# Kernel tuning notes

Measured on AMD Instinct MI355X. Metric: run time of the kernel, lower is better.

## Reference

```python
import jax, jax.numpy as jnp
import numpy as np

H = 64          # hidden_dim
EP = 60000      # edges per relation type; block order: nmos, pmos, R, L, C
E = 5 * EP
N_IN = 50000
N_OUT = 50000


def _gelu(x):
    return jax.nn.gelu(x, approximate=False)  # torch nn.GELU default = exact erf


def _mlp_blocked(x, Ws, bs):
    # x: [T, N, Din]; independent MLP per relation-type block; GELU after all but last layer
    for i, (W, b) in enumerate(zip(Ws, bs)):
        x = jnp.einsum('tnd,tdh->tnh', x, W) + b[:, None, :]
        if i < len(Ws) - 1:
            x = _gelu(x)
    return x


def _mlp(x, Ws, bs):
    for i, (W, b) in enumerate(zip(Ws, bs)):
        x = x @ W + b
        if i < len(Ws) - 1:
            x = _gelu(x)
    return x


def _segment_softmax(logits, seg, num_seg):
    # torch_geometric-style softmax: normalized per dst-node segment, per feature column
    m = jax.ops.segment_max(logits, seg, num_segments=num_seg)
    ex = jnp.exp(logits - m[seg])
    den = jax.ops.segment_sum(ex, seg, num_segments=num_seg)
    return ex / den[seg]


def _forward(floats, src_types, dst_types, src_nodes, dst_nodes,
             vg_types, vg_idx, vb_types, vb_idx, n_output_nodes):
    (input_voltages, device_params, nf1_W, nf1_b,
     ef1_W1, ef1_b1, ef1_W2, ef1_b2, ef1_W3, ef1_b3,
     ef2m_W1, ef2m_b1, ef2m_W2, ef2m_b2, ef2m_W3, ef2m_b3, ef2m_W4, ef2m_b4,
     ef2r_W1, ef2r_b1, ef2r_W2, ef2r_b2, ef2r_W3, ef2r_b3, ef2r_W4, ef2r_b4,
     self_W1, self_b1, self_W2, self_b2, self_W3, self_b3, self_W4, self_b4,
     score_W, score_b) = floats
    # ef1: per-relation-type 3-layer MLP on the scalar device parameter -> [E, H]
    ef1 = _mlp_blocked(device_params,
                       [ef1_W1, ef1_W2, ef1_W3],
                       [ef1_b1, ef1_b2, ef1_b3]).reshape(E, H)
    nf1_input = input_voltages[:, None] @ nf1_W + nf1_b           # [N_IN, H]
    # (ef1 @ ef1.T)[dst_out] @ ef1 == ef1[dst_out] @ (ef1.T @ ef1) -- avoids the E x E matrix
    logits = ef1 @ (ef1.T @ ef1)                                  # [E, H]
    # edges whose dst is not an 'output' node go to a dump segment that is dropped
    seg = jnp.where(dst_types == 1, dst_nodes, n_output_nodes)
    att = _segment_softmax(logits, seg, n_output_nodes + 1)
    nf1_output = jax.ops.segment_sum(att * ef1, seg,
                                     num_segments=n_output_nodes + 1)[:n_output_nodes]

    def pick(types, idx):
        # node_types.index: 0 -> 'input' table, 1 -> 'output' table
        return jnp.where((types == 0)[:, None], nf1_input[idx], nf1_output[idx])

    nf1_src = pick(src_types, src_nodes)
    nf1_dst = pick(dst_types, dst_nodes)
    nf1_vg = pick(vg_types, vg_idx)     # gate node feats (mos edges only) [2*EP, H]
    nf1_vb = pick(vb_types, vb_idx)     # bulk node feats (mos edges only) [2*EP, H]

    M = 2 * EP
    x_mos = jnp.concatenate([ef1[:M], nf1_src[:M], nf1_dst[:M], nf1_vg, nf1_vb], -1).reshape(2, EP, 5 * H)
    x_rlc = jnp.concatenate([ef1[M:], nf1_src[M:], nf1_dst[M:]], -1).reshape(3, EP, 3 * H)
    ef2_mos = _mlp_blocked(x_mos, [ef2m_W1, ef2m_W2, ef2m_W3, ef2m_W4],
                           [ef2m_b1, ef2m_b2, ef2m_b3, ef2m_b4])
    ef2_rlc = _mlp_blocked(x_rlc, [ef2r_W1, ef2r_W2, ef2r_W3, ef2r_W4],
                           [ef2r_b1, ef2r_b2, ef2r_b3, ef2r_b4])
    ef2 = jnp.concatenate([ef2_mos.reshape(M, H), ef2_rlc.reshape(3 * EP, H)], 0)
    ef2 = ef2 + _mlp(ef1, [self_W1, self_W2, self_W3, self_W4],
                     [self_b1, self_b2, self_b3, self_b4])
    return ef2 @ score_W + score_b                                # [E, H]


def setup_inputs():
    key = jax.random.key(0)
    ks = iter(jax.random.split(key, 64))

    def nrm(shape, s):
        return jax.random.normal(next(ks), shape, jnp.float32) * s

    def ri(shape, hi):
        return jax.random.randint(next(ks), shape, 0, hi, jnp.int32)

    w = 0.1  # ~ xavier-normal scale for these fan-ins
    return {
        'input_voltages': nrm([N_IN], 1.0),
        'device_params': nrm([5, EP, 1], 1.0),
        'src_types': ri([E], 2), 'dst_types': ri([E], 2),
        'src_nodes': ri([E], N_IN), 'dst_nodes': ri([E], N_OUT),
        'vg_types': ri([2 * EP], 2), 'vg_idx': ri([2 * EP], N_IN),
        'vb_types': ri([2 * EP], 2), 'vb_idx': ri([2 * EP], N_IN),
        'n_output_nodes': N_OUT,
        'nf1_W': nrm([1, H], w), 'nf1_b': nrm([H], w),
        'ef1_W1': nrm([5, 1, H], w), 'ef1_b1': nrm([5, H], w),
        'ef1_W2': nrm([5, H, H], w), 'ef1_b2': nrm([5, H], w),
        'ef1_W3': nrm([5, H, H], w), 'ef1_b3': nrm([5, H], w),
        'ef2m_W1': nrm([2, 5 * H, H], 0.05), 'ef2m_b1': nrm([2, H], w),
        'ef2m_W2': nrm([2, H, H], w), 'ef2m_b2': nrm([2, H], w),
        'ef2m_W3': nrm([2, H, H], w), 'ef2m_b3': nrm([2, H], w),
        'ef2m_W4': nrm([2, H, H], w), 'ef2m_b4': nrm([2, H], w),
        'ef2r_W1': nrm([3, 3 * H, H], 0.05), 'ef2r_b1': nrm([3, H], w),
        'ef2r_W2': nrm([3, H, H], w), 'ef2r_b2': nrm([3, H], w),
        'ef2r_W3': nrm([3, H, H], w), 'ef2r_b3': nrm([3, H], w),
        'ef2r_W4': nrm([3, H, H], w), 'ef2r_b4': nrm([3, H], w),
        'self_W1': nrm([H, H], w), 'self_b1': nrm([H], w),
        'self_W2': nrm([H, H], w), 'self_b2': nrm([H], w),
        'self_W3': nrm([H, H], w), 'self_b3': nrm([H], w),
        'self_W4': nrm([H, H], w), 'self_b4': nrm([H], w),
        'score_W': nrm([H, H], w), 'score_b': nrm([H], w),
    }


def reference(input_voltages, device_params, src_types, dst_types, src_nodes, dst_nodes,
              vg_types, vg_idx, vb_types, vb_idx, n_output_nodes,
              nf1_W, nf1_b,
              ef1_W1, ef1_b1, ef1_W2, ef1_b2, ef1_W3, ef1_b3,
              ef2m_W1, ef2m_b1, ef2m_W2, ef2m_b2, ef2m_W3, ef2m_b3, ef2m_W4, ef2m_b4,
              ef2r_W1, ef2r_b1, ef2r_W2, ef2r_b2, ef2r_W3, ef2r_b3, ef2r_W4, ef2r_b4,
              self_W1, self_b1, self_W2, self_b2, self_W3, self_b3, self_W4, self_b4,
              score_W, score_b):
    floats = (input_voltages, device_params, nf1_W, nf1_b,
              ef1_W1, ef1_b1, ef1_W2, ef1_b2, ef1_W3, ef1_b3,
              ef2m_W1, ef2m_b1, ef2m_W2, ef2m_b2, ef2m_W3, ef2m_b3, ef2m_W4, ef2m_b4,
              ef2r_W1, ef2r_b1, ef2r_W2, ef2r_b2, ef2r_W3, ef2r_b3, ef2r_W4, ef2r_b4,
              self_W1, self_b1, self_W2, self_b2, self_W3, self_b3, self_W4, self_b4,
              score_W, score_b)
    return _forward(floats, src_types, dst_types, src_nodes, dst_nodes,
                    vg_types, vg_idx, vb_types, vb_idx, n_output_nodes)
```

## Files before the change

kernel.cpp:

```cpp
#include <hip/hip_runtime.h>
#include <hip/hip_bf16.h>

#define EP 60000
#define NE 300000
#define M2 120000
#define NIN 50000
#define NOUT 50000
#define PAD 65
#define NIMG 49
#define GP 72

typedef __bf16 b16x8 __attribute__((ext_vector_type(8)));
typedef float f32x4 __attribute__((ext_vector_type(4)));
typedef unsigned short us8 __attribute__((ext_vector_type(8)));
typedef unsigned short us4 __attribute__((ext_vector_type(4)));

__device__ __forceinline__ float gelu_f(float x) {
    return 0.5f * x * (1.0f + erff(x * 0.70710678118654752440f));
}

__device__ __forceinline__ float gelu_fast(float x) {
    float ax = fabsf(x) * 0.70710678118654752440f;
    float t = __builtin_amdgcn_rcpf(fmaf(0.3275911f, ax, 1.0f));
    float y = fmaf(fmaf(fmaf(fmaf(1.061405429f, t, -1.453152027f), t, 1.421413741f),
                        t, -0.284496736f), t, 0.254829592f) * t;
    float e = __expf(-ax * ax);
    float erf = fmaf(-y, e, 1.0f);
    return 0.5f * x * (1.0f + copysignf(erf, x));
}

__device__ __forceinline__ unsigned short bfhi(float f) {
    unsigned int u = __float_as_uint(f);
    u += 0x7FFFu + ((u >> 16) & 1u);
    return (unsigned short)(u >> 16);
}

__device__ __forceinline__ void split2(float f, unsigned short& h, unsigned short& l) {
    h = bfhi(f);
    float fh = __uint_as_float(((unsigned int)h) << 16);
    l = bfhi(f - fh);
}

__device__ __forceinline__ void split2f(float f, unsigned short& h, unsigned short& l) {
    unsigned int u = __float_as_uint(f);
    h = (unsigned short)(u >> 16);
    float fh = __uint_as_float(u & 0xFFFF0000u);
    l = bfhi(f - fh);
}

__device__ __forceinline__ float bf2f(unsigned short u) {
    return __uint_as_float(((unsigned int)u) << 16);
}

__device__ __forceinline__ int xidx(int row, int col) {
    return (row * 64 + col) ^ ((row & 7) << 3);
}

__device__ __forceinline__ b16x8 ldfrag(const unsigned short* p, int id) {
    return __builtin_bit_cast(b16x8, *(const us8*)(p + id));
}

__device__ __forceinline__ f32x4 MF(b16x8 a, b16x8 b, f32x4 c) {
    return __builtin_amdgcn_mfma_f32_16x16x32_bf16(a, b, c, 0, 0, 0);
}

__device__ __forceinline__ void zacc(f32x4 a[2][2]) {
#pragma unroll
    for (int i = 0; i < 2; ++i)
#pragma unroll
        for (int j = 0; j < 2; ++j) a[i][j] = (f32x4){0.f, 0.f, 0.f, 0.f};
}

__device__ __forceinline__ void gll16(const unsigned short* g, unsigned short* l) {
    __builtin_amdgcn_global_load_lds((const __attribute__((address_space(1))) void*)g,
                                     (__attribute__((address_space(3))) void*)l, 16, 0, 0);
}

__device__ __forceinline__ void stageWimg(const unsigned short* __restrict__ img,
                                          unsigned short* __restrict__ WHL, int tid) {
    int w = tid >> 6, lane = tid & 63;
#pragma unroll
    for (int j = 0; j < 2; ++j)
        gll16(img + w * 1024 + j * 512 + lane * 8, WHL + w * 1024 + j * 512);
}

__device__ __forceinline__ void stageX_rows(const unsigned short* __restrict__ src, int rmax,
                                            unsigned short* __restrict__ XH, unsigned short* __restrict__ XL,
                                            int tid) {
#pragma unroll
    for (int q = 0; q < 4; ++q) {
        int f = q * 512 + tid;
        int row = f >> 4, cc = f & 15;
        int rc = min(row, rmax - 1);
        us8 v = *(const us8*)(src + (size_t)rc * 128 + cc * 8);
        unsigned short* pl = (cc < 8) ? XH : XL;
        *(us8*)(pl + xidx(row, (cc & 7) * 8)) = v;
    }
}

__device__ __forceinline__ void stageX_pick(const int* __restrict__ tp, const int* __restrict__ ix, int base,
                                            int rmax, const float* __restrict__ volt,
                                            const unsigned short* __restrict__ nfo,
                                            const float* __restrict__ sNW, const float* __restrict__ sNB,
                                            unsigned short* __restrict__ XH, unsigned short* __restrict__ XL,
                                            int tid) {
#pragma unroll
    for (int q = 0; q < 4; ++q) {
        int f = q * 512 + tid;
        int row = f >> 4, cc = f & 15;
        int rc = min(row, rmax - 1);
        int ty = tp[base + rc];
        int idx = ix[base + rc];
        int c8 = (cc & 7) * 8;
        unsigned short* pl = (cc < 8) ? XH : XL;
        us8 v;
        if (ty == 0) {
            float vv = volt[idx];
#pragma unroll
            for (int j = 0; j < 8; ++j) {
                float x = fmaf(vv, sNW[c8 + j], sNB[c8 + j]);
                unsigned short h, l;
                split2f(x, h, l);
                v[j] = (cc < 8) ? h : l;
            }
        } else {
            v = *(const us8*)(nfo + (size_t)idx * 128 + cc * 8);
        }
        *(us8*)(pl + xidx(row, c8)) = v;
    }
}

__device__ __forceinline__ void mf_gemm64(const unsigned short* __restrict__ XH, const unsigned short* __restrict__ XL,
                                          const unsigned short* __restrict__ WH, const unsigned short* __restrict__ WL,
                                          f32x4 acc[2][2], int wr, int wc, int lane) {
    int lr = lane & 15, g = lane >> 4;
#pragma unroll
    for (int kk = 0; kk < 2; ++kk) {
        int k0 = kk * 32 + g * 8;
        b16x8 ah[2], al[2];
#pragma unroll
        for (int rt = 0; rt < 2; ++rt) {
            int id = xidx(wr * 32 + rt * 16 + lr, k0);
            ah[rt] = ldfrag(XH, id);
            al[rt] = ldfrag(XL, id);
        }
#pragma unroll
        for (int t = 0; t < 2; ++t) {
            int id = xidx((wc * 2 + t) * 16 + lr, k0);
            b16x8 bh = ldfrag(WH, id), bl = ldfrag(WL, id);
#pragma unroll
            for (int rt = 0; rt < 2; ++rt) {
                acc[rt][t] = MF(ah[rt], bh, acc[rt][t]);
                acc[rt][t] = MF(ah[rt], bl, acc[rt][t]);
                acc[rt][t] = MF(al[rt], bh, acc[rt][t]);
            }
        }
    }
}

template <bool GELU, bool FAST>
__device__ __forceinline__ void writeback(f32x4 acc[2][2], const float* __restrict__ sb,
                                          unsigned short* __restrict__ XH, unsigned short* __restrict__ XL,
                                          int wr, int wc, int lane) {
    int lr = lane & 15, g = lane >> 4;
#pragma unroll
    for (int rt = 0; rt < 2; ++rt)
#pragma unroll
        for (int t = 0; t < 2; ++t)
#pragma unroll
            for (int r = 0; r < 4; ++r) {
                int row = wr * 32 + rt * 16 + g * 4 + r;
                int col = (wc * 2 + t) * 16 + lr;
                float v = acc[rt][t][r] + sb[col];
                if (GELU) v = FAST ? gelu_fast(v) : gelu_f(v);
                unsigned short h, l;
                if (FAST) split2f(v, h, l); else split2(v, h, l);
                int id = xidx(row, col);
                XH[id] = h; XL[id] = l;
            }
}

__device__ __forceinline__ void writeglob(f32x4 acc[2][2], const float* __restrict__ sb,
                                          float* __restrict__ dst, int rmax, int wr, int wc, int lane) {
    int lr = lane & 15, g = lane >> 4;
#pragma unroll
    for (int rt = 0; rt < 2; ++rt)
#pragma unroll
        for (int t = 0; t < 2; ++t)
#pragma unroll
            for (int r = 0; r < 4; ++r) {
                int row = wr * 32 + rt * 16 + g * 4 + r;
                if (row < rmax) {
                    int col = (wc * 2 + t) * 16 + lr;
                    dst[(size_t)row * 64 + col] = acc[rt][t][r] + sb[col];
                }
            }
}

__device__ __forceinline__ void writeglob_split(f32x4 acc[2][2], const float* __restrict__ sb,
                                                unsigned short* __restrict__ dst, int rmax,
                                                int wr, int wc, int lane) {
    int lr = lane & 15, g = lane >> 4;
#pragma unroll
    for (int rt = 0; rt < 2; ++rt)
#pragma unroll
        for (int t = 0; t < 2; ++t)
#pragma unroll
            for (int r = 0; r < 4; ++r) {
                int row = wr * 32 + rt * 16 + g * 4 + r;
                if (row < rmax) {
                    int col = (wc * 2 + t) * 16 + lr;
                    float v = acc[rt][t][r] + sb[col];
                    unsigned short h, l;
                    split2(v, h, l);
                    dst[(size_t)row * 128 + col] = h;
                    dst[(size_t)row * 128 + 64 + col] = l;
                }
            }
}

__global__ void k_zero(int* __restrict__ p, int n) {
    int i = blockIdx.x * 256 + threadIdx.x;
    if (i < n) p[i] = 0;
}

__global__ __launch_bounds__(256) void k_prepw(
    const float* __restrict__ e1W2, const float* __restrict__ e1W3,
    const float* __restrict__ mW1, const float* __restrict__ mW2,
    const float* __restrict__ mW3, const float* __restrict__ mW4,
    const float* __restrict__ rW1, const float* __restrict__ rW2,
    const float* __restrict__ rW3, const float* __restrict__ rW4,
    const float* __restrict__ sw1, const float* __restrict__ sw2,
    const float* __restrict__ sw3, const float* __restrict__ sw4,
    const float* __restrict__ scw, unsigned short* __restrict__ wimg) {
    int b = blockIdx.x, tid = threadIdx.x;
    const float* src;
    if (b < 5) src = e1W2 + b * 4096;
    else if (b < 10) src = e1W3 + (b - 5) * 4096;
    else if (b < 20) src = mW1 + (b - 10) * 4096;
    else if (b < 22) src = mW2 + (b - 20) * 4096;
    else if (b < 24) src = mW3 + (b - 22) * 4096;
    else if (b < 26) src = mW4 + (b - 24) * 4096;
    else if (b < 35) src = rW1 + (b - 26) * 4096;
    else if (b < 38) src = rW2 + (b - 35) * 4096;
    else if (b < 41) src = rW3 + (b - 38) * 4096;
    else if (b < 44) src = rW4 + (b - 41) * 4096;
    else if (b == 44) src = sw1;
    else if (b == 45) src = sw2;
    else if (b == 46) src = sw3;
    else if (b == 47) src = sw4;
    else src = scw;
    unsigned short* dst = wimg + (size_t)b * 8192;
#pragma unroll
    for (int q = 0; q < 4; ++q) {
        int flat = q * 256 + tid;
        int k = flat >> 4, n4 = (flat & 15) * 4;
        float4 v = ((const float4*)src)[flat];
        float vv[4] = {v.x, v.y, v.z, v.w};
#pragma unroll
        for (int i = 0; i < 4; ++i) {
            unsigned short h, l;
            split2(vv[i], h, l);
            int id = xidx(n4 + i, k);
            dst[id] = h;
            dst[4096 + id] = l;
        }
    }
}

__global__ __launch_bounds__(512, 4) void k_ef1(
    const float* __restrict__ dp,
    const float* __restrict__ w1, const float* __restrict__ b1,
    const float* __restrict__ b2, const float* __restrict__ b3,
    const unsigned short* __restrict__ wimg,
    unsigned short* __restrict__ e1s) {
    __shared__ unsigned short XH[8192], XL[8192], WHL[8192];
    __shared__ float sb[2][64], sW1[64], sB1[64];
    const int tid = threadIdx.x, ty = blockIdx.y;
    const int i0 = blockIdx.x * 128;
    const int rmax = min(128, EP - i0);
    const int w = tid >> 6, lane = tid & 63;
    const int wr = w >> 1, wc = w & 1;
    const size_t row0 = (size_t)ty * EP + i0;

    stageWimg(wimg + (size_t)ty * 8192, WHL, tid);
    if (tid < 64) { sW1[tid] = w1[ty * 64 + tid]; sB1[tid] = b1[ty * 64 + tid]; }
    else if (tid < 128) sb[0][tid - 64] = b2[ty * 64 + tid - 64];
    else if (tid < 192) sb[1][tid - 128] = b3[ty * 64 + tid - 128];
    __syncthreads();
#pragma unroll
    for (int q = 0; q < 4; ++q) {
        int flat = q * 512 + tid;
        int rr = flat >> 4, cc = flat & 15;
        int rc = min(rr, rmax - 1);
        float d = dp[(size_t)ty * EP + i0 + rc];
        us4 h, l;
#pragma unroll
        for (int j = 0; j < 4; ++j) {
            int c = cc * 4 + j;
            float v = gelu_f(fmaf(d, sW1[c], sB1[c]));
            unsigned short hh, ll;
            split2(v, hh, ll);
            h[j] = hh; l[j] = ll;
        }
        *(us4*)(XH + xidx(rr, cc * 4)) = h;
        *(us4*)(XL + xidx(rr, cc * 4)) = l;
    }
    __syncthreads();
    f32x4 acc[2][2];
    zacc(acc); mf_gemm64(XH, XL, WHL, WHL + 4096, acc, wr, wc, lane);
    __syncthreads();
    writeback<true, false>(acc, sb[0], XH, XL, wr, wc, lane);
    stageWimg(wimg + (size_t)(5 + ty) * 8192, WHL, tid);
    __syncthreads();
    zacc(acc); mf_gemm64(XH, XL, WHL, WHL + 4096, acc, wr, wc, lane);
    writeglob_split(acc, sb[1], e1s + row0 * 128, rmax, wr, wc, lane);
}

__device__ __forceinline__ void zero16(float* a) {
#pragma unroll
    for (int q = 0; q < 16; ++q) a[q] = 0.f;
}

__device__ __forceinline__ void stage4k(const float* __restrict__ g, float* __restrict__ l) {
    const float4* g4 = (const float4*)g;
    float4* l4 = (float4*)l;
    int t = threadIdx.x;
#pragma unroll
    for (int q = 0; q < 4; ++q) l4[q * 256 + t] = g4[q * 256 + t];
}

__device__ __forceinline__ void tile_gemm(const float* __restrict__ xt, const float* __restrict__ Wl,
                                          float* __restrict__ acc, int r, int c4) {
    const float4* W4 = (const float4*)Wl;
#pragma unroll 8
    for (int k = 0; k < 64; ++k) {
        float xv = xt[r * PAD + k];
#pragma unroll
        for (int q = 0; q < 4; ++q) {
            float4 w = W4[k * 16 + c4 + q];
            acc[q * 4 + 0] = fmaf(xv, w.x, acc[q * 4 + 0]);
            acc[q * 4 + 1] = fmaf(xv, w.y, acc[q * 4 + 1]);
            acc[q * 4 + 2] = fmaf(xv, w.z, acc[q * 4 + 2]);
            acc[q * 4 + 3] = fmaf(xv, w.w, acc[q * 4 + 3]);
        }
    }
}

__global__ __launch_bounds__(256) void k_gram(const unsigned short* __restrict__ e1s, float* __restrict__ G) {
    __shared__ unsigned short TH[64 * GP], TL[64 * GP];
    const int tid = threadIdx.x;
    const int wv = tid >> 6, lane = tid & 63;
    const int lr = lane & 15, g = lane >> 4;
    f32x4 acc[4];
#pragma unroll
    for (int t = 0; t < 4; ++t) acc[t] = (f32x4){0.f, 0.f, 0.f, 0.f};
    const int nchk = (NE + 63) >> 6;
    for (int ch = blockIdx.x; ch < nchk; ch += gridDim.x) {
        int r0 = ch * 64;
        __syncthreads();
#pragma unroll
        for (int q = 0; q < 4; ++q) {
            int f = q * 256 + tid;
            int pl = f >> 9, rem = f & 511;
            int row = rem >> 3, cc = rem & 7;
            int rr = r0 + row;
            us8 v = (us8){0, 0, 0, 0, 0, 0, 0, 0};
            if (rr < NE) v = *(const us8*)(e1s + (size_t)rr * 128 + pl * 64 + cc * 8);
            unsigned short* dstp = pl ? TL : TH;
#pragma unroll
            for (int j = 0; j < 8; ++j) dstp[(cc * 8 + j) * GP + row] = v[j];
        }
        __syncthreads();
#pragma unroll
        for (int kk = 0; kk < 2; ++kk) {
            int k0 = kk * 32 + g * 8;
            b16x8 ah = ldfrag(TH, (wv * 16 + lr) * GP + k0);
            b16x8 al = ldfrag(TL, (wv * 16 + lr) * GP + k0);
#pragma unroll
            for (int b = 0; b < 4; ++b) {
                b16x8 bh = ldfrag(TH, (b * 16 + lr) * GP + k0);
                b16x8 bl = ldfrag(TL, (b * 16 + lr) * GP + k0);
                acc[b] = MF(ah, bh, acc[b]);
                acc[b] = MF(ah, bl, acc[b]);
                acc[b] = MF(al, bh, acc[b]);
            }
        }
    }
#pragma unroll
    for (int b = 0; b < 4; ++b)
#pragma unroll
        for (int r = 0; r < 4; ++r) {
            int row = wv * 16 + g * 4 + r;
            int col = b * 16 + lr;
            atomicAdd(&G[row * 64 + col], acc[b][r]);
        }
}

__global__ void k_hist(const int* __restrict__ dst_t, const int* __restrict__ dst_n, int* __restrict__ hist) {
    int e = blockIdx.x * 256 + threadIdx.x;
    if (e < NE && dst_t[e] == 1) atomicAdd(&hist[dst_n[e]], 1);
}

__global__ __launch_bounds__(1024) void k_scan(const int* __restrict__ hist, int* __restrict__ row_start) {
    __shared__ int part[1024];
    const int tid = threadIdx.x;
    const int chunk = (NOUT + 1023) / 1024;
    int lo = tid * chunk, hi = min(lo + chunk, NOUT);
    int s = 0;
    for (int i = lo; i < hi; ++i) s += hist[i];
    part[tid] = s;
    __syncthreads();
    for (int off = 1; off < 1024; off <<= 1) {
        int v = part[tid];
        int add = (tid >= off) ? part[tid - off] : 0;
        __syncthreads();
        part[tid] = v + add;
        __syncthreads();
    }
    int base = (tid == 0) ? 0 : part[tid - 1];
    for (int i = lo; i < hi; ++i) { row_start[i] = base; base += hist[i]; }
    if (lo < NOUT && hi == NOUT) row_start[NOUT] = base;
}

__global__ void k_scatter(const int* __restrict__ dst_t, const int* __restrict__ dst_n,
                          const int* __restrict__ row_start, int* __restrict__ cursor, int* __restrict__ elist) {
    int e = blockIdx.x * 256 + threadIdx.x;
    if (e < NE && dst_t[e] == 1) {
        int n = dst_n[e];
        int pos = atomicAdd(&cursor[n], 1);
        elist[row_start[n] + pos] = e;
    }
}

__global__ __launch_bounds__(256) void k_logits_c(const unsigned short* __restrict__ e1s,
                                                  const float* __restrict__ G,
                                                  const int* __restrict__ row_start,
                                                  const int* __restrict__ elist,
                                                  float* __restrict__ lgc) {
    __shared__ float A[64 * PAD], Wb[4096];
    const int tid = threadIdx.x;
    const int NV = row_start[NOUT];
    const int i0 = blockIdx.x * 64;
    if (i0 >= NV) return;
    const int rmax = min(64, NV - i0);
    const int r = tid & 63, c0 = (tid >> 6) * 16, c4 = c0 >> 2;
    stage4k(G, Wb);
#pragma unroll
    for (int q = 0; q < 4; ++q) {
        int flat = q * 256 + tid;
        int rr = flat >> 4, cc = flat & 15;
        int rc = min(rr, rmax - 1);
        int eid = elist[i0 + rc];
        const unsigned short* rp = e1s + (size_t)eid * 128;
        us4 h = *(const us4*)(rp + cc * 4);
        us4 l = *(const us4*)(rp + 64 + cc * 4);
        float* d = &A[rr * PAD + cc * 4];
#pragma unroll
        for (int j = 0; j < 4; ++j) d[j] = bf2f(h[j]) + bf2f(l[j]);
    }
    __syncthreads();
    float acc[16];
    zero16(acc); tile_gemm(A, Wb, acc, r, c4);
    if (r < rmax) {
        float* dst = lgc + (size_t)(i0 + r) * 64;
#pragma unroll
        for (int q = 0; q < 4; ++q)
            ((float4*)dst)[c4 + q] =
                make_float4(acc[q * 4 + 0], acc[q * 4 + 1], acc[q * 4 + 2], acc[q * 4 + 3]);
    }
}

__global__ __launch_bounds__(256) void k_att(const float* __restrict__ lgc, const unsigned short* __restrict__ e1s,
                                             const int* __restrict__ row_start, const int* __restrict__ elist,
                                             unsigned short* __restrict__ nfo) {
    int n = blockIdx.x * 4 + (threadIdx.x >> 6);
    int lane = threadIdx.x & 63;
    if (n >= NOUT) return;
    int s = row_start[n], t = row_start[n + 1];
    float m = -3.0e38f, den = 0.f, num = 0.f;
    for (int i = s; i < t; ++i) {
        int eid = elist[i];
        float x = lgc[(size_t)i * 64 + lane];
        float e = bf2f(e1s[(size_t)eid * 128 + lane]) + bf2f(e1s[(size_t)eid * 128 + 64 + lane]);
        float mn = fmaxf(m, x);
        float sc = __expf(m - mn);
        float ex = __expf(x - mn);
        den = fmaf(den, sc, ex);
        num = fmaf(num, sc, ex * e);
        m = mn;
    }
    float v = (t > s) ? num / den : 0.f;
    unsigned short h, l;
    split2(v, h, l);
    nfo[(size_t)n * 128 + lane] = h;
    nfo[(size_t)n * 128 + 64 + lane] = l;
}

__global__ __launch_bounds__(512, 4) void k_fuse(
    const unsigned short* __restrict__ e1s, const unsigned short* __restrict__ nfo,
    const unsigned short* __restrict__ wimg, const float* __restrict__ volt,
    const int* __restrict__ src_t, const int* __restrict__ src_n,
    const int* __restrict__ dst_t, const int* __restrict__ dst_n,
    const int* __restrict__ vg_t, const int* __restrict__ vg_i,
    const int* __restrict__ vb_t, const int* __restrict__ vb_i,
    const float* __restrict__ nf1W, const float* __restrict__ nf1b,
    const float* __restrict__ mb1, const float* __restrict__ mb2,
    const float* __restrict__ mb3, const float* __restrict__ mb4,
    const float* __restrict__ rb1, const float* __restrict__ rb2,
    const float* __restrict__ rb3, const float* __restrict__ rb4,
    const float* __restrict__ selb1, const float* __restrict__ selb2,
    const float* __restrict__ selb3, const float* __restrict__ selb4,
    const float* __restrict__ scb, float* __restrict__ out) {
    __shared__ unsigned short XH[8192], XL[8192], WHL[8192];
    __shared__ float sb[3][64], sNW[64], sNB[64];
    const int tid = threadIdx.x;
    const int gy = blockIdx.y;
    const bool mos = gy < 2;
    const int ty = mos ? gy : gy - 2;
    const int nch = mos ? 5 : 3;
    const int i0 = blockIdx.x * 128;
    const int rmax = min(128, EP - i0);
    const int w = tid >> 6, lane = tid & 63;
    const int wr = w >> 1, wc = w & 1;
    const int lr = lane & 15;
    const int erow0 = (mos ? 0 : M2) + ty * EP + i0;
    const int w1base = mos ? 10 + ty * 5 : 26 + ty * 3;
    const int w2img = mos ? 20 + ty : 35 + ty;
    const int w3img = mos ? 22 + ty : 38 + ty;
    const int w4img = mos ? 24 + ty : 41 + ty;
    const float* b1 = mos ? mb1 : rb1;
    const float* b2 = mos ? mb2 : rb2;
    const float* b3 = mos ? mb3 : rb3;
    const float* b4 = mos ? mb4 : rb4;

    stageWimg(wimg + (size_t)44 * 8192, WHL, tid);
    stageX_rows(e1s + (size_t)erow0 * 128, rmax, XH, XL, tid);
    if (tid < 64) sNW[tid] = nf1W[tid];
    else if (tid < 128) sNB[tid - 64] = nf1b[tid - 64];
    else if (tid < 192) sb[0][tid - 128] = b1[ty * 64 + tid - 128];
    __syncthreads();

    f32x4 acc[2][2], accS[2][2], ef2r[2][2];
    zacc(accS);
    mf_gemm64(XH, XL, WHL, WHL + 4096, accS, wr, wc, lane);
    __syncthreads();
    stageWimg(wimg + (size_t)w1base * 8192, WHL, tid);
    __syncthreads();
    zacc(acc);
    mf_gemm64(XH, XL, WHL, WHL + 4096, acc, wr, wc, lane);
    for (int c = 1; c < nch; ++c) {
        __syncthreads();
        stageWimg(wimg + (size_t)(w1base + c) * 8192, WHL, tid);
        if (c == 1) stageX_pick(src_t, src_n, erow0, rmax, volt, nfo, sNW, sNB, XH, XL, tid);
        else if (c == 2) stageX_pick(dst_t, dst_n, erow0, rmax, volt, nfo, sNW, sNB, XH, XL, tid);
        else if (c == 3) stageX_pick(vg_t, vg_i, erow0, rmax, volt, nfo, sNW, sNB, XH, XL, tid);
        else stageX_pick(vb_t, vb_i, erow0, rmax, volt, nfo, sNW, sNB, XH, XL, tid);
        __syncthreads();
        mf_gemm64(XH, XL, WHL, WHL + 4096, acc, wr, wc, lane);
    }
    __syncthreads();
    writeback<true, true>(acc, sb[0], XH, XL, wr, wc, lane);
    stageWimg(wimg + (size_t)w2img * 8192, WHL, tid);
    if (tid < 64) sb[1][tid] = b2[ty * 64 + tid];
    __syncthreads();
    zacc(acc); mf_gemm64(XH, XL, WHL, WHL + 4096, acc, wr, wc, lane);
    __syncthreads();
    writeback<true, true>(acc, sb[1], XH, XL, wr, wc, lane);
    stageWimg(wimg + (size_t)w3img * 8192, WHL, tid);
    if (tid < 64) sb[2][tid] = b3[ty * 64 + tid];
    __syncthreads();
    zacc(acc); mf_gemm64(XH, XL, WHL, WHL + 4096, acc, wr, wc, lane);
    __syncthreads();
    writeback<true, true>(acc, sb[2], XH, XL, wr, wc, lane);
    stageWimg(wimg + (size_t)w4img * 8192, WHL, tid);
    if (tid < 64) sb[0][tid] = b4[ty * 64 + tid];
    else if (tid < 128) sb[1][tid - 64] = selb1[tid - 64];
    __syncthreads();
    zacc(acc); mf_gemm64(XH, XL, WHL, WHL + 4096, acc, wr, wc, lane);
#pragma unroll
    for (int rt = 0; rt < 2; ++rt)
#pragma unroll
        for (int t = 0; t < 2; ++t)
#pragma unroll
            for (int r = 0; r < 4; ++r)
                ef2r[rt][t][r] = acc[rt][t][r] + sb[0][(wc * 2 + t) * 16 + lr];
    __syncthreads();
    writeback<true, true>(accS, sb[1], XH, XL, wr, wc, lane);
    stageWimg(wimg + (size_t)45 * 8192, WHL, tid);
    if (tid < 64) sb[2][tid] = selb2[tid];
    __syncthreads();
    zacc(acc); mf_gemm64(XH, XL, WHL, WHL + 4096, acc, wr, wc, lane);
    __syncthreads();
    writeback<true, true>(acc, sb[2], XH, XL, wr, wc, lane);
    stageWimg(wimg + (size_t)46 * 8192, WHL, tid);
    if (tid < 64) sb[0][tid] = selb3[tid];
    __syncthreads();
    zacc(acc); mf_gemm64(XH, XL, WHL, WHL + 4096, acc, wr, wc, lane);
    __syncthreads();
    writeback<true, true>(acc, sb[0], XH, XL, wr, wc, lane);
    stageWimg(wimg + (size_t)47 * 8192, WHL, tid);
    if (tid < 64) sb[1][tid] = selb4[tid];
    __syncthreads();
    zacc(acc); mf_gemm64(XH, XL, WHL, WHL + 4096, acc, wr, wc, lane);
    __syncthreads();
    {
        int g = lane >> 4;
#pragma unroll
        for (int rt = 0; rt < 2; ++rt)
#pragma unroll
            for (int t = 0; t < 2; ++t)
#pragma unroll
                for (int r = 0; r < 4; ++r) {
                    int row = wr * 32 + rt * 16 + g * 4 + r;
                    int col = (wc * 2 + t) * 16 + lr;
                    float v = acc[rt][t][r] + sb[1][col] + ef2r[rt][t][r];
                    unsigned short h, l;
                    split2f(v, h, l);
                    int id = xidx(row, col);
                    XH[id] = h; XL[id] = l;
                }
    }
    stageWimg(wimg + (size_t)48 * 8192, WHL, tid);
    if (tid < 64) sb[2][tid] = scb[tid];
    __syncthreads();
    zacc(acc); mf_gemm64(XH, XL, WHL, WHL + 4096, acc, wr, wc, lane);
    writeglob(acc, sb[2], out + (size_t)erow0 * 64, rmax, wr, wc, lane);
}

extern "C" void kernel_launch(void* const* d_in, const int* in_sizes, int n_in,
                              void* d_out, int out_size, void* d_ws, size_t ws_size,
                              hipStream_t stream) {
    const float* volt = (const float*)d_in[0];
    const float* dp   = (const float*)d_in[1];
    const int* src_t  = (const int*)d_in[2];
    const int* dst_t  = (const int*)d_in[3];
    const int* src_n  = (const int*)d_in[4];
    const int* dst_n  = (const int*)d_in[5];
    const int* vg_t   = (const int*)d_in[6];
    const int* vg_i   = (const int*)d_in[7];
    const int* vb_t   = (const int*)d_in[8];
    const int* vb_i   = (const int*)d_in[9];
    const float* nf1W = (const float*)d_in[11];
    const float* nf1b = (const float*)d_in[12];
    const float* e1W1 = (const float*)d_in[13];
    const float* e1b1 = (const float*)d_in[14];
    const float* e1W2 = (const float*)d_in[15];
    const float* e1b2 = (const float*)d_in[16];
    const float* e1W3 = (const float*)d_in[17];
    const float* e1b3 = (const float*)d_in[18];
    const float* mW1 = (const float*)d_in[19];  const float* mb1 = (const float*)d_in[20];
    const float* mW2 = (const float*)d_in[21];  const float* mb2 = (const float*)d_in[22];
    const float* mW3 = (const float*)d_in[23];  const float* mb3 = (const float*)d_in[24];
    const float* mW4 = (const float*)d_in[25];  const float* mb4 = (const float*)d_in[26];
    const float* rW1 = (const float*)d_in[27];  const float* rb1 = (const float*)d_in[28];
    const float* rW2 = (const float*)d_in[29];  const float* rb2 = (const float*)d_in[30];
    const float* rW3 = (const float*)d_in[31];  const float* rb3 = (const float*)d_in[32];
    const float* rW4 = (const float*)d_in[33];  const float* rb4 = (const float*)d_in[34];
    const float* selW1 = (const float*)d_in[35]; const float* selb1 = (const float*)d_in[36];
    const float* selW2 = (const float*)d_in[37]; const float* selb2 = (const float*)d_in[38];
    const float* selW3 = (const float*)d_in[39]; const float* selb3 = (const float*)d_in[40];
    const float* selW4 = (const float*)d_in[41]; const float* selb4 = (const float*)d_in[42];
    const float* scW = (const float*)d_in[43];   const float* scb = (const float*)d_in[44];

    float* lgc = (float*)d_ws;
    unsigned short* NFO  = (unsigned short*)(lgc + (size_t)NE * 64);
    unsigned short* WIMG = NFO + (size_t)NOUT * 128;
    float* G = (float*)(WIMG + (size_t)NIMG * 8192);
    int* hist      = (int*)(G + 4096);
    int* cursor    = hist + NOUT;
    int* row_start = cursor + NOUT;
    int* elist     = row_start + NOUT + 1;
    unsigned short* E1S = (unsigned short*)d_out;

    const int T128_EP = (EP + 127) / 128;
    const int TILES_E = (NE + 63) / 64;
    dim3 b256(256), b512(512);

    k_prepw<<<NIMG, b256, 0, stream>>>(e1W2, e1W3, mW1, mW2, mW3, mW4,
                                       rW1, rW2, rW3, rW4, selW1, selW2, selW3, selW4, scW, WIMG);
    {
        int nz = 4096 + NOUT + NOUT;
        k_zero<<<(nz + 255) / 256, b256, 0, stream>>>((int*)G, nz);
    }
    k_ef1<<<dim3(T128_EP, 5), b512, 0, stream>>>(dp, e1W1, e1b1, e1b2, e1b3, WIMG, E1S);
    k_hist<<<(NE + 255) / 256, b256, 0, stream>>>(dst_t, dst_n, hist);
    k_scan<<<1, 1024, 0, stream>>>(hist, row_start);
    k_scatter<<<(NE + 255) / 256, b256, 0, stream>>>(dst_t, dst_n, row_start, cursor, elist);
    k_gram<<<640, b256, 0, stream>>>(E1S, G);
    k_logits_c<<<TILES_E, b256, 0, stream>>>(E1S, G, row_start, elist, lgc);
    k_att<<<NOUT / 4, b256, 0, stream>>>(lgc, E1S, row_start, elist, NFO);
    k_fuse<<<dim3(T128_EP, 5), b512, 0, stream>>>(E1S, NFO, WIMG, volt,
        src_t, src_n, dst_t, dst_n, vg_t, vg_i, vb_t, vb_i, nf1W, nf1b,
        mb1, mb2, mb3, mb4, rb1, rb2, rb3, rb4,
        selb1, selb2, selb3, selb4, scb, (float*)d_out);
}
```

Before: 414.1 us.

## Move attention logits GEMM to MFMA with split-bf16 Gram matrix image

Replaces the scalar FP32 tile GEMM in the logits kernel with the MFMA split-bf16 GEMM path already used elsewhere. A new small kernel converts the Gram matrix into the hi/lo bf16 weight image layout, and the logits kernel now uses 128-row tiles with 512 threads, gathering edge rows through the sorted edge list. It also swaps several split2 calls for a split2f variant. This adds a kernel launch and relies on split-bf16 accuracy being sufficient for the softmax logits.

```diff
diff --git a/kernel.cpp b/kernel.cpp
--- a/kernel.cpp
+++ b/kernel.cpp
@@ -8,6 +8,7 @@
 #define NOUT 50000
 #define PAD 65
 #define NIMG 49
+#define GIMG_ID 49
 #define GP 72
 
 typedef __bf16 b16x8 __attribute__((ext_vector_type(8)));
@@ -93,6 +94,22 @@
         int row = f >> 4, cc = f & 15;
         int rc = min(row, rmax - 1);
         us8 v = *(const us8*)(src + (size_t)rc * 128 + cc * 8);
+        unsigned short* pl = (cc < 8) ? XH : XL;
+        *(us8*)(pl + xidx(row, (cc & 7) * 8)) = v;
+    }
+}
+
+__device__ __forceinline__ void stageX_elist(const unsigned short* __restrict__ e1s,
+                                             const int* __restrict__ elist, int base, int rmax,
+                                             unsigned short* __restrict__ XH, unsigned short* __restrict__ XL,
+                                             int tid) {
+#pragma unroll
+    for (int q = 0; q < 4; ++q) {
+        int f = q * 512 + tid;
+        int row = f >> 4, cc = f & 15;
+        int rc = min(row, rmax - 1);
+        int eid = elist[base + rc];
+        us8 v = *(const us8*)(e1s + (size_t)eid * 128 + cc * 8);
         unsigned short* pl = (cc < 8) ? XH : XL;
         *(us8*)(pl + xidx(row, (cc & 7) * 8)) = v;
     }
@@ -197,6 +214,23 @@
             }
 }
 
+__device__ __forceinline__ void writeglob_nb(f32x4 acc[2][2], float* __restrict__ dst,
+                                             int rmax, int wr, int wc, int lane) {
+    int lr = lane & 15, g = lane >> 4;
+#pragma unroll
+    for (int rt = 0; rt < 2; ++rt)
+#pragma unroll
+        for (int t = 0; t < 2; ++t)
+#pragma unroll
+            for (int r = 0; r < 4; ++r) {
+                int row = wr * 32 + rt * 16 + g * 4 + r;
+                if (row < rmax) {
+                    int col = (wc * 2 + t) * 16 + lr;
+                    dst[(size_t)row * 64 + col] = acc[rt][t][r];
+                }
+            }
+}
+
 __device__ __forceinline__ void writeglob_split(f32x4 acc[2][2], const float* __restrict__ sb,
                                                 unsigned short* __restrict__ dst, int rmax,
                                                 int wr, int wc, int lane) {
@@ -212,7 +246,7 @@
                     int col = (wc * 2 + t) * 16 + lr;
                     float v = acc[rt][t][r] + sb[col];
                     unsigned short h, l;
-                    split2(v, h, l);
+                    split2f(v, h, l);
                     dst[(size_t)row * 128 + col] = h;
                     dst[(size_t)row * 128 + 64 + col] = l;
                 }
@@ -268,6 +302,27 @@
     }
 }
 
+__global__ __launch_bounds__(256) void k_prepg(const float* __restrict__ G,
+                                               unsigned short* __restrict__ wimg) {
+    int tid = threadIdx.x;
+    unsigned short* dst = wimg + (size_t)GIMG_ID * 8192;
+#pragma unroll
+    for (int q = 0; q < 4; ++q) {
+        int flat = q * 256 + tid;
+        int k = flat >> 4, n4 = (flat & 15) * 4;
+        float4 v = ((const float4*)G)[flat];
+        float vv[4] = {v.x, v.y, v.z, v.w};
+#pragma unroll
+        for (int i = 0; i < 4; ++i) {
+            unsigned short h, l;
+            split2(vv[i], h, l);
+            int id = xidx(n4 + i, k);
+            dst[id] = h;
+            dst[4096 + id] = l;
+        }
+    }
+}
+
 __global__ __launch_bounds__(512, 4) void k_ef1(
     const float* __restrict__ dp,
     const float* __restrict__ w1, const float* __restrict__ b1,
@@ -300,7 +355,7 @@
             int c = cc * 4 + j;
             float v = gelu_f(fmaf(d, sW1[c], sB1[c]));
             unsigned short hh, ll;
-            split2(v, hh, ll);
+            split2f(v, hh, ll);
             h[j] = hh; l[j] = ll;
         }
         *(us4*)(XH + xidx(rr, cc * 4)) = h;
@@ -315,36 +370,6 @@
     __syncthreads();
     zacc(acc); mf_gemm64(XH, XL, WHL, WHL + 4096, acc, wr, wc, lane);
     writeglob_split(acc, sb[1], e1s + row0 * 128, rmax, wr, wc, lane);
-}
-
-__device__ __forceinline__ void zero16(float* a) {
-#pragma unroll
-    for (int q = 0; q < 16; ++q) a[q] = 0.f;
-}
-
-__device__ __forceinline__ void stage4k(const float* __restrict__ g, float* __restrict__ l) {
-    const float4* g4 = (const float4*)g;
-    float4* l4 = (float4*)l;
-    int t = threadIdx.x;
-#pragma unroll
-    for (int q = 0; q < 4; ++q) l4[q * 256 + t] = g4[q * 256 + t];
-}
-
-__device__ __forceinline__ void tile_gemm(const float* __restrict__ xt, const float* __restrict__ Wl,
-                                          float* __restrict__ acc, int r, int c4) {
-    const float4* W4 = (const float4*)Wl;
-#pragma unroll 8
-    for (int k = 0; k < 64; ++k) {
-        float xv = xt[r * PAD + k];
-#pragma unroll
-        for (int q = 0; q < 4; ++q) {
-            float4 w = W4[k * 16 + c4 + q];
-            acc[q * 4 + 0] = fmaf(xv, w.x, acc[q * 4 + 0]);
-            acc[q * 4 + 1] = fmaf(xv, w.y, acc[q * 4 + 1]);
-            acc[q * 4 + 2] = fmaf(xv, w.z, acc[q * 4 + 2]);
-            acc[q * 4 + 3] = fmaf(xv, w.w, acc[q * 4 + 3]);
-        }
-    }
 }
 
 __global__ __launch_bounds__(256) void k_gram(const unsigned short* __restrict__ e1s, float* __restrict__ G) {
@@ -433,42 +458,26 @@
     }
 }
 
-__global__ __launch_bounds__(256) void k_logits_c(const unsigned short* __restrict__ e1s,
-                                                  const float* __restrict__ G,
-                                                  const int* __restrict__ row_start,
-                                                  const int* __restrict__ elist,
-                                                  float* __restrict__ lgc) {
-    __shared__ float A[64 * PAD], Wb[4096];
+__global__ __launch_bounds__(512, 4) void k_logits_c(const unsigned short* __restrict__ e1s,
+                                                     const unsigned short* __restrict__ wimg,
+                                                     const int* __restrict__ row_start,
+                                                     const int* __restrict__ elist,
+                                                     float* __restrict__ lgc) {
+    __shared__ unsigned short XH[8192], XL[8192], WHL[8192];
     const int tid = threadIdx.x;
     const int NV = row_start[NOUT];
-    const int i0 = blockIdx.x * 64;
+    const int i0 = blockIdx.x * 128;
     if (i0 >= NV) return;
-    const int rmax = min(64, NV - i0);
-    const int r = tid & 63, c0 = (tid >> 6) * 16, c4 = c0 >> 2;
-    stage4k(G, Wb);
-#pragma unroll
-    for (int q = 0; q < 4; ++q) {
-        int flat = q * 256 + tid;
-        int rr = flat >> 4, cc = flat & 15;
-        int rc = min(rr, rmax - 1);
-        int eid = elist[i0 + rc];
-        const unsigned short* rp = e1s + (size_t)eid * 128;
-        us4 h = *(const us4*)(rp + cc * 4);
-        us4 l = *(const us4*)(rp + 64 + cc * 4);
-        float* d = &A[rr * PAD + cc * 4];
-#pragma unroll
-        for (int j = 0; j < 4; ++j) d[j] = bf2f(h[j]) + bf2f(l[j]);
-    }
-    __syncthreads();
-    float acc[16];
-    zero16(acc); tile_gemm(A, Wb, acc, r, c4);
-    if (r < rmax) {
-        float* dst = lgc + (size_t)(i0 + r) * 64;
-#pragma unroll
-        for (int q = 0; q < 4; ++q)
-            ((float4*)dst)[c4 + q] =
-                make_float4(acc[q * 4 + 0], acc[q * 4 + 1], acc[q * 4 + 2], acc[q * 4 + 3]);
-    }
+    const int rmax = min(128, NV - i0);
+    const int w = tid >> 6, lane = tid & 63;
+    const int wr = w >> 1, wc = w & 1;
+
+    stageWimg(wimg + (size_t)GIMG_ID * 8192, WHL, tid);
+    stageX_elist(e1s, elist, i0, rmax, XH, XL, tid);
+    __syncthreads();
+    f32x4 acc[2][2];
+    zacc(acc); mf_gemm64(XH, XL, WHL, WHL + 4096, acc, wr, wc, lane);
+    writeglob_nb(acc, lgc + (size_t)i0 * 64, rmax, wr, wc, lane);
 }
 
 __global__ __launch_bounds__(256) void k_att(const float* __restrict__ lgc, const unsigned short* __restrict__ e1s,
@@ -492,7 +501,7 @@
     }
     float v = (t > s) ? num / den : 0.f;
     unsigned short h, l;
-    split2(v, h, l);
+    split2f(v, h, l);
     nfo[(size_t)n * 128 + lane] = h;
     nfo[(size_t)n * 128 + 64 + lane] = l;
 }
@@ -666,7 +675,7 @@
     float* lgc = (float*)d_ws;
     unsigned short* NFO  = (unsigned short*)(lgc + (size_t)NE * 64);
     unsigned short* WIMG = NFO + (size_t)NOUT * 128;
-    float* G = (float*)(WIMG + (size_t)NIMG * 8192);
+    float* G = (float*)(WIMG + (size_t)(NIMG + 1) * 8192);
     int* hist      = (int*)(G + 4096);
     int* cursor    = hist + NOUT;
     int* row_start = cursor + NOUT;
@@ -674,7 +683,7 @@
     unsigned short* E1S = (unsigned short*)d_out;
 
     const int T128_EP = (EP + 127) / 128;
-    const int TILES_E = (NE + 63) / 64;
+    const int T128_E  = (NE + 127) / 128;
     dim3 b256(256), b512(512);
 
     k_prepw<<<NIMG, b256, 0, stream>>>(e1W2, e1W3, mW1, mW2, mW3, mW4,
@@ -688,7 +697,8 @@
     k_scan<<<1, 1024, 0, stream>>>(hist, row_start);
     k_scatter<<<(NE + 255) / 256, b256, 0, stream>>>(dst_t, dst_n, row_start, cursor, elist);
     k_gram<<<640, b256, 0, stream>>>(E1S, G);
-    k_logits_c<<<TILES_E, b256, 0, stream>>>(E1S, G, row_start, elist, lgc);
+    k_prepg<<<1, b256, 0, stream>>>(G, WIMG);
+    k_logits_c<<<T128_E, b512, 0, stream>>>(E1S, WIMG, row_start, elist, lgc);
     k_att<<<NOUT / 4, b256, 0, stream>>>(lgc, E1S, row_start, elist, NFO);
     k_fuse<<<dim3(T128_EP, 5), b512, 0, stream>>>(E1S, NFO, WIMG, volt,
         src_t, src_n, dst_t, dst_n, vg_t, vg_i, vb_t, vb_i, nf1W, nf1b,
```

After: 412.2 us. About the same (-0.5%).
